# Optimization experiments

Measured on AMD Instinct MI355X. Metric: run time of the kernel, lower is better.

## Reference

```python
import jax, jax.numpy as jnp
import numpy as np

N = 50000   # total nodes in batched graph
E = 400000  # directed edges
G = 512     # number of graphs in batch
F = 128     # input node feature dim
K = 4       # attention heads
H = 64      # hidden feats per head (flatten width = K*H = 256)
EPS = 1e-5  # BatchNorm eps


def _edge_softmax(e, dst, n):
    # softmax of per-edge scores over incoming edges of each dst node; e: [E, K]
    m = jax.ops.segment_max(e, dst, num_segments=n)
    ee = jnp.exp(e - m[dst])
    s = jax.ops.segment_sum(ee, dst, num_segments=n)
    return ee / s[dst]


def _gat_layer(x, W, al, ar, b, resW, src, dst, agg):
    # dgl GATConv with residual=True, LeakyReLU(0.2), bias, ReLU activation
    n = x.shape[0]
    z = (x @ W).reshape(n, K, H)                      # [N, K, H]
    el = jnp.einsum('nkh,kh->nk', z, al)              # [N, K]
    er = jnp.einsum('nkh,kh->nk', z, ar)
    e = jax.nn.leaky_relu(el[src] + er[dst], negative_slope=0.2)  # [E, K]
    a = _edge_softmax(e, dst, n)                      # [E, K]
    rst = jax.ops.segment_sum(a[:, :, None] * z[src], dst, num_segments=n)  # [N, K, H]
    res = (x @ resW).reshape(n, K, H) if resW is not None else x.reshape(n, K, H)
    rst = jax.nn.relu(rst + res + b.reshape(1, K, H))
    return rst.reshape(n, K * H) if agg == 'flatten' else rst.mean(axis=1)


def setup_inputs() -> dict:
    key = jax.random.key(0)
    ks = jax.random.split(key, 16)
    f32 = jnp.float32

    def p(k, shape):
        return jax.random.normal(k, shape, f32) * 0.1

    h = jax.random.normal(ks[0], (N, F), f32)
    src = jax.random.randint(ks[1], (E,), 0, N)
    dst = jax.random.randint(ks[2], (E,), 0, N)
    graph_ids = (jnp.arange(N) * G) // N  # sorted node->graph assignment, all segments nonempty

    return dict(
        h=h, src=src, dst=dst, graph_ids=graph_ids,
        W0=p(ks[3], (F, K * H)), al0=p(ks[4], (K, H)), ar0=p(ks[5], (K, H)),
        b0=jnp.zeros((K * H,), f32), resW0=p(ks[6], (F, K * H)),
        W1=p(ks[7], (K * H, K * H)), al1=p(ks[8], (K, H)), ar1=p(ks[9], (K, H)),
        b1=jnp.zeros((K * H,), f32),
        W2=p(ks[10], (K * H, K * H)), al2=p(ks[11], (K, H)), ar2=p(ks[12], (K, H)),
        b2=jnp.zeros((K * H,), f32),
        Wg=p(ks[13], (H, 1)), bg=jnp.zeros((1,), f32),
        Wm1=p(ks[14], (2 * H, H)), bm1=jnp.zeros((H,), f32),
        bn_g=jnp.ones((H,), f32), bn_b=jnp.zeros((H,), f32),
        bn_m=jnp.zeros((H,), f32), bn_v=jnp.ones((H,), f32),
        Wm2=p(ks[15], (H, 1)), bm2=jnp.zeros((1,), f32),
    )


def reference(h, src, dst, graph_ids, W0, al0, ar0, b0, resW0, W1, al1, ar1, b1,
              W2, al2, ar2, b2, Wg, bg, Wm1, bm1, bn_g, bn_b, bn_m, bn_v, Wm2, bm2):
    # 3 GAT layers: flatten, flatten, mean (dgllife GATPredictor default agg modes)
    x = _gat_layer(h, W0, al0, ar0, b0, resW0, src, dst, 'flatten')   # [N, 256]
    x = _gat_layer(x, W1, al1, ar1, b1, None, src, dst, 'flatten')    # [N, 256] (identity residual)
    x = _gat_layer(x, W2, al2, ar2, b2, None, src, dst, 'mean')       # [N, 64]
    # WeightedSumAndMax readout
    w = jax.nn.sigmoid(x @ Wg + bg)                                   # [N, 1]
    gs = jax.ops.segment_sum(w * x, graph_ids, num_segments=G)        # [G, 64]
    gm = jax.ops.segment_max(x, graph_ids, num_segments=G)            # [G, 64]
    gf = jnp.concatenate([gs, gm], axis=1)                            # [G, 128]
    # MLPPredictor (eval mode: dropout off, BatchNorm uses running stats)
    y = jax.nn.relu(gf @ Wm1 + bm1)
    y = (y - bn_m) / jnp.sqrt(bn_v + EPS) * bn_g + bn_b
    out = jax.nn.sigmoid(y @ Wm2 + bm2)                               # [G, 1]
    return out
```

## Files before the change

kernel.cpp:

```cpp
#include <hip/hip_runtime.h>
#include <math.h>


typedef _Float16 f16;
typedef _Float16 f16x4 __attribute__((ext_vector_type(4)));
typedef _Float16 f16x8 __attribute__((ext_vector_type(8)));
typedef float f32x16 __attribute__((ext_vector_type(16)));

__device__ __forceinline__ double wred_sumd(double v) {
#pragma unroll
  for (int m = 32; m > 0; m >>= 1) v += __shfl_xor(v, m, 64);
  return v;
}
__device__ __forceinline__ float wred_sum(float v) {
#pragma unroll
  for (int m = 32; m > 0; m >>= 1) v += __shfl_xor(v, m, 64);
  return v;
}

__global__ void k_hist(const int* __restrict__ dst, int* __restrict__ deg, int e) {
  int i = blockIdx.x * 256 + threadIdx.x;
  if (i < e) atomicAdd(&deg[dst[i]], 1);
}

__global__ void k_scan1(const int* __restrict__ deg, int* __restrict__ rowptr,
                        int* __restrict__ bsum, int n) {
  __shared__ int sh[256];
  int t = threadIdx.x;
  int base = blockIdx.x * 1024 + t * 4;
  int v0 = 0, v1 = 0, v2 = 0, v3 = 0;
  if (base + 0 < n) v0 = deg[base + 0];
  if (base + 1 < n) v1 = deg[base + 1];
  if (base + 2 < n) v2 = deg[base + 2];
  if (base + 3 < n) v3 = deg[base + 3];
  sh[t] = v0 + v1 + v2 + v3;
  __syncthreads();
  for (int off = 1; off < 256; off <<= 1) {
    int x = (t >= off) ? sh[t - off] : 0;
    __syncthreads();
    sh[t] += x;
    __syncthreads();
  }
  int excl = (t > 0) ? sh[t - 1] : 0;
  if (base + 0 < n) rowptr[base + 0] = excl;
  if (base + 1 < n) rowptr[base + 1] = excl + v0;
  if (base + 2 < n) rowptr[base + 2] = excl + v0 + v1;
  if (base + 3 < n) rowptr[base + 3] = excl + v0 + v1 + v2;
  if (t == 255) bsum[blockIdx.x] = sh[255];
}

__global__ void k_scan2(int* bsum, int nb) {
  if (threadIdx.x == 0 && blockIdx.x == 0) {
    int run = 0;
    for (int i = 0; i < nb; i++) { int v = bsum[i]; bsum[i] = run; run += v; }
  }
}

__global__ void k_scan3(int* __restrict__ rowptr, const int* __restrict__ bsum,
                        int n, int e) {
  int i = blockIdx.x * 256 + threadIdx.x;
  if (i < n) rowptr[i] += bsum[i >> 10];
  if (i == 0) rowptr[n] = e;
}

__global__ void k_scatter(const int* __restrict__ src, const int* __restrict__ dst,
                          const int* __restrict__ rowptr, int* __restrict__ cursor,
                          int* __restrict__ colsrc, int e) {
  int i = blockIdx.x * 256 + threadIdx.x;
  if (i < e) {
    int d = dst[i];
    int pos = rowptr[d] + atomicAdd(&cursor[d], 1);
    colsrc[pos] = src[i];
  }
}

__global__ __launch_bounds__(256) void k_split(const float* __restrict__ X,
                                               f16* __restrict__ X0,
                                               f16* __restrict__ X1, int n4) {
  int i = blockIdx.x * 256 + threadIdx.x;
  if (i >= n4) return;
  float4 v = *(const float4*)(X + (size_t)i * 4);
  f16x4 hi, lo;
  hi.x = (f16)v.x; lo.x = (f16)(v.x - (float)hi.x);
  hi.y = (f16)v.y; lo.y = (f16)(v.y - (float)hi.y);
  hi.z = (f16)v.z; lo.z = (f16)(v.z - (float)hi.z);
  hi.w = (f16)v.w; lo.w = (f16)(v.w - (float)hi.w);
  *(f16x4*)(X0 + (size_t)i * 4) = hi;
  *(f16x4*)(X1 + (size_t)i * 4) = lo;
}

__global__ void k_splitWT(const float* __restrict__ W, f16* __restrict__ P0,
                          f16* __restrict__ P1, int kin) {
  int c = blockIdx.x;
  for (int k = threadIdx.x; k < kin; k += blockDim.x) {
    float v = W[(size_t)k * 256 + c];
    f16 h0 = (f16)v;
    size_t off = ((size_t)(k >> 4) * 256 + c) * 16 + ((k >> 3) & 1) * 8 + (k & 7);
    P0[off] = h0;
    P1[off] = (f16)(v - (float)h0);
  }
}

template <int KIN>
__global__ __launch_bounds__(256) void k_gemm_mfma(
    const f16* __restrict__ X0, const f16* __restrict__ X1,
    const f16* __restrict__ WT0, const f16* __restrict__ WT1,
    float* __restrict__ C, int M) {
  __shared__ f16 aLDS[2][2][64][8];
  const int t = threadIdx.x;
  const int w = t >> 6;
  const int lane = t & 63;
  const int lo = lane & 31, g = lane >> 5;
  const int row0 = blockIdx.x * 32;

  f32x16 acc0, acc1;
#pragma unroll
  for (int i = 0; i < 16; i++) { acc0[i] = 0.f; acc1[i] = 0.f; }

  const size_t fb0 = (size_t)(w * 64 + lo) * 16 + g * 8;
  const size_t fb1 = (size_t)(w * 64 + 32 + lo) * 16 + g * 8;

  for (int k0 = 0; k0 < KIN; k0 += 32) {
    if (k0) __syncthreads();
    {
      int s = t >> 7, r = (t >> 2) & 31, hh = t & 3;
      int kh = hh >> 1, gg = hh & 1;
      int gr = row0 + r;
      if (gr > M - 1) gr = M - 1;
      const f16* Xs = s ? X1 : X0;
      *(float4*)&aLDS[s][kh][(gg << 5) | r][0] =
          *(const float4*)&Xs[(size_t)gr * KIN + k0 + kh * 16 + gg * 8];
    }
    __syncthreads();
#pragma unroll
    for (int kh = 0; kh < 2; kh++) {
      const size_t bbase = (size_t)((k0 >> 4) + kh) * 4096;
      f16x8 a0 = *(const f16x8*)&aLDS[0][kh][lane][0];
      f16x8 a1 = *(const f16x8*)&aLDS[1][kh][lane][0];
      f16x8 b0c0 = *(const f16x8*)&WT0[bbase + fb0];
      f16x8 b0c1 = *(const f16x8*)&WT0[bbase + fb1];
      f16x8 b1c0 = *(const f16x8*)&WT1[bbase + fb0];
      f16x8 b1c1 = *(const f16x8*)&WT1[bbase + fb1];
      acc0 = __builtin_amdgcn_mfma_f32_32x32x16_f16(a0, b0c0, acc0, 0, 0, 0);
      acc1 = __builtin_amdgcn_mfma_f32_32x32x16_f16(a0, b0c1, acc1, 0, 0, 0);
      acc0 = __builtin_amdgcn_mfma_f32_32x32x16_f16(a0, b1c0, acc0, 0, 0, 0);
      acc1 = __builtin_amdgcn_mfma_f32_32x32x16_f16(a0, b1c1, acc1, 0, 0, 0);
      acc0 = __builtin_amdgcn_mfma_f32_32x32x16_f16(a1, b0c0, acc0, 0, 0, 0);
      acc1 = __builtin_amdgcn_mfma_f32_32x32x16_f16(a1, b0c1, acc1, 0, 0, 0);
    }
  }
  const int c0 = w * 64 + lo, c1 = w * 64 + 32 + lo;
#pragma unroll
  for (int reg = 0; reg < 16; reg++) {
    int rr = (reg & 3) + 8 * (reg >> 2) + 4 * g;
    int r0 = row0 + rr;
    if (r0 < M) {
      C[(size_t)r0 * 256 + c0] = acc0[reg];
      C[(size_t)r0 * 256 + c1] = acc1[reg];
    }
  }
}

__global__ __launch_bounds__(256) void k_elr(const float* __restrict__ z,
                                             const float* __restrict__ al,
                                             const float* __restrict__ ar,
                                             float* __restrict__ el,
                                             float* __restrict__ er, int n) {
  int node = blockIdx.x * 4 + (threadIdx.x >> 6);
  int lane = threadIdx.x & 63;
  if (node >= n) return;
  const float* zr = z + (size_t)node * 256;
#pragma unroll
  for (int k = 0; k < 4; k++) {
    float zv = zr[k * 64 + lane];
    float pl = wred_sum(zv * al[k * 64 + lane]);
    float pr = wred_sum(zv * ar[k * 64 + lane]);
    if (lane == 0) {
      el[node * 4 + k] = pl;
      er[node * 4 + k] = pr;
    }
  }
}

template <int MEAN, int RESF16>
__global__ __launch_bounds__(256) void k_gather(
    const float* __restrict__ z, const float* __restrict__ el,
    const float* __restrict__ er, const float* __restrict__ resf,
    const f16* __restrict__ R0, const f16* __restrict__ R1,
    const float* __restrict__ bias, const int* __restrict__ rowptr,
    const int* __restrict__ colsrc, float* __restrict__ out,
    f16* __restrict__ O0, f16* __restrict__ O1, float* __restrict__ wn,
    const float* __restrict__ Wg, const float* __restrict__ bg, int n) {
  const int t = threadIdx.x;
  const int w = t >> 6, lane = t & 63;
  int node = blockIdx.x * 4 + w;
  if (node > n - 1) node = n - 1;
  const int base = rowptr[node];
  const int deg = rowptr[node + 1] - base;
  const int k = lane >> 4, j = lane & 15;
  const float ernk = er[node * 4 + k];

  float m = -INFINITY;
  for (int i0 = 0; i0 < deg; i0 += 16) {
    int i = i0 + j;
    if (i < deg) {
      int s = colsrc[base + i];
      float sc = el[s * 4 + k] + ernk;
      sc = (sc > 0.f) ? sc : 0.2f * sc;
      m = fmaxf(m, sc);
    }
  }
#pragma unroll
  for (int msk = 1; msk < 16; msk <<= 1) m = fmaxf(m, __shfl_xor(m, msk, 64));

  float ssum = 0.f;
  for (int i0 = 0; i0 < deg; i0 += 16) {
    int i = i0 + j;
    if (i < deg) {
      int s = colsrc[base + i];
      float sc = el[s * 4 + k] + ernk;
      sc = (sc > 0.f) ? sc : 0.2f * sc;
      ssum += expf(sc - m);
    }
  }
#pragma unroll
  for (int msk = 1; msk < 16; msk <<= 1) ssum += __shfl_xor(ssum, msk, 64);
  const float inv = 1.f / ssum;

  const char* zb = (const char*)z + lane * 16;
  float4 acc0 = {0, 0, 0, 0}, acc1 = {0, 0, 0, 0};
  float4 acc2 = {0, 0, 0, 0}, acc3 = {0, 0, 0, 0};
  int i = 0;
  for (; i + 4 <= deg; i += 4) {
    int s0 = colsrc[base + i + 0];
    int s1 = colsrc[base + i + 1];
    int s2 = colsrc[base + i + 2];
    int s3 = colsrc[base + i + 3];
    float4 z0 = *(const float4*)(zb + ((size_t)s0 << 10));
    float4 z1 = *(const float4*)(zb + ((size_t)s1 << 10));
    float4 z2 = *(const float4*)(zb + ((size_t)s2 << 10));
    float4 z3 = *(const float4*)(zb + ((size_t)s3 << 10));
    float c0 = el[s0 * 4 + k] + ernk; c0 = (c0 > 0.f) ? c0 : 0.2f * c0;
    float c1 = el[s1 * 4 + k] + ernk; c1 = (c1 > 0.f) ? c1 : 0.2f * c1;
    float c2 = el[s2 * 4 + k] + ernk; c2 = (c2 > 0.f) ? c2 : 0.2f * c2;
    float c3 = el[s3 * 4 + k] + ernk; c3 = (c3 > 0.f) ? c3 : 0.2f * c3;
    float a0 = expf(c0 - m) * inv;
    float a1 = expf(c1 - m) * inv;
    float a2 = expf(c2 - m) * inv;
    float a3 = expf(c3 - m) * inv;
    acc0.x = fmaf(a0, z0.x, acc0.x); acc0.y = fmaf(a0, z0.y, acc0.y);
    acc0.z = fmaf(a0, z0.z, acc0.z); acc0.w = fmaf(a0, z0.w, acc0.w);
    acc1.x = fmaf(a1, z1.x, acc1.x); acc1.y = fmaf(a1, z1.y, acc1.y);
    acc1.z = fmaf(a1, z1.z, acc1.z); acc1.w = fmaf(a1, z1.w, acc1.w);
    acc2.x = fmaf(a2, z2.x, acc2.x); acc2.y = fmaf(a2, z2.y, acc2.y);
    acc2.z = fmaf(a2, z2.z, acc2.z); acc2.w = fmaf(a2, z2.w, acc2.w);
    acc3.x = fmaf(a3, z3.x, acc3.x); acc3.y = fmaf(a3, z3.y, acc3.y);
    acc3.z = fmaf(a3, z3.z, acc3.z); acc3.w = fmaf(a3, z3.w, acc3.w);
  }
  for (; i < deg; i++) {
    int s = colsrc[base + i];
    float4 zv = *(const float4*)(zb + ((size_t)s << 10));
    float c = el[s * 4 + k] + ernk; c = (c > 0.f) ? c : 0.2f * c;
    float av = expf(c - m) * inv;
    acc0.x = fmaf(av, zv.x, acc0.x); acc0.y = fmaf(av, zv.y, acc0.y);
    acc0.z = fmaf(av, zv.z, acc0.z); acc0.w = fmaf(av, zv.w, acc0.w);
  }

  size_t o = (size_t)node * 256 + lane * 4;
  float4 rv;
  if (RESF16) {
    f16x4 rh = *(const f16x4*)(R0 + o);
    f16x4 rl = *(const f16x4*)(R1 + o);
    rv.x = (float)rh.x + (float)rl.x;
    rv.y = (float)rh.y + (float)rl.y;
    rv.z = (float)rh.z + (float)rl.z;
    rv.w = (float)rh.w + (float)rl.w;
  } else {
    rv = *(const float4*)(resf + o);
  }
  float4 bv = *(const float4*)(bias + lane * 4);
  float4 v;
  v.x = fmaxf(((acc0.x + acc1.x) + (acc2.x + acc3.x)) + rv.x + bv.x, 0.f);
  v.y = fmaxf(((acc0.y + acc1.y) + (acc2.y + acc3.y)) + rv.y + bv.y, 0.f);
  v.z = fmaxf(((acc0.z + acc1.z) + (acc2.z + acc3.z)) + rv.z + bv.z, 0.f);
  v.w = fmaxf(((acc0.w + acc1.w) + (acc2.w + acc3.w)) + rv.w + bv.w, 0.f);

  if (!MEAN) {
    f16x4 hi, lo;
    hi.x = (f16)v.x; lo.x = (f16)(v.x - (float)hi.x);
    hi.y = (f16)v.y; lo.y = (f16)(v.y - (float)hi.y);
    hi.z = (f16)v.z; lo.z = (f16)(v.z - (float)hi.z);
    hi.w = (f16)v.w; lo.w = (f16)(v.w - (float)hi.w);
    *(f16x4*)(O0 + o) = hi;
    *(f16x4*)(O1 + o) = lo;
  } else {
    __shared__ float tmp[4][256];
    *(float4*)&tmp[w][lane * 4] = v;
    __syncthreads();
    float xv = 0.25f * (tmp[w][lane] + tmp[w][lane + 64] + tmp[w][lane + 128] +
                        tmp[w][lane + 192]);
    out[(size_t)node * 64 + lane] = xv;
    double s = wred_sumd((double)xv * (double)Wg[lane]);
    if (lane == 0)
      wn[node] = (float)(1.0 / (1.0 + exp(-(s + (double)bg[0]))));
  }
}

__global__ __launch_bounds__(64) void k_readout(const float* __restrict__ x2,
                                                const float* __restrict__ wn,
                                                float* __restrict__ gf, int n,
                                                int g) {
  int gi = blockIdx.x;
  int lane = threadIdx.x;
  long long start = ((long long)gi * n + g - 1) / g;
  long long end = ((long long)(gi + 1) * n + g - 1) / g;
  double s = 0.0;
  float mx = -INFINITY;
  for (long long nd = start; nd < end; nd++) {
    float xv = x2[nd * 64 + lane];
    s += (double)wn[nd] * (double)xv;
    mx = fmaxf(mx, xv);
  }
  gf[gi * 128 + lane] = (float)s;
  gf[gi * 128 + 64 + lane] = mx;
}

__global__ __launch_bounds__(64) void k_mlp(const float* __restrict__ gf,
                                            const float* __restrict__ Wm1,
                                            const float* __restrict__ bm1,
                                            const float* __restrict__ bng,
                                            const float* __restrict__ bnb,
                                            const float* __restrict__ bnm,
                                            const float* __restrict__ bnv,
                                            const float* __restrict__ Wm2,
                                            const float* __restrict__ bm2,
                                            float* __restrict__ out) {
  int gi = blockIdx.x;
  int h = threadIdx.x;
  double y = (double)bm1[h];
  for (int i = 0; i < 128; i++)
    y += (double)gf[gi * 128 + i] * (double)Wm1[i * 64 + h];
  y = (y > 0.0) ? y : 0.0;
  y = (y - (double)bnm[h]) / sqrt((double)bnv[h] + 1e-5) * (double)bng[h] +
      (double)bnb[h];
  double v = wred_sumd(y * (double)Wm2[h]);
  if (h == 0) {
    double s = v + (double)bm2[0];
    out[gi] = (float)(1.0 / (1.0 + exp(-s)));
  }
}

extern "C" void kernel_launch(void* const* d_in, const int* in_sizes, int n_in,
                              void* d_out, int out_size, void* d_ws,
                              size_t ws_size, hipStream_t stream) {
  const float* h    = (const float*)d_in[0];
  const int*   src  = (const int*)d_in[1];
  const int*   dst  = (const int*)d_in[2];
  const float* W0    = (const float*)d_in[4];
  const float* al0   = (const float*)d_in[5];
  const float* ar0   = (const float*)d_in[6];
  const float* b0    = (const float*)d_in[7];
  const float* resW0 = (const float*)d_in[8];
  const float* W1    = (const float*)d_in[9];
  const float* al1   = (const float*)d_in[10];
  const float* ar1   = (const float*)d_in[11];
  const float* b1    = (const float*)d_in[12];
  const float* W2    = (const float*)d_in[13];
  const float* al2   = (const float*)d_in[14];
  const float* ar2   = (const float*)d_in[15];
  const float* b2    = (const float*)d_in[16];
  const float* Wg    = (const float*)d_in[17];
  const float* bg    = (const float*)d_in[18];
  const float* Wm1   = (const float*)d_in[19];
  const float* bm1   = (const float*)d_in[20];
  const float* bng   = (const float*)d_in[21];
  const float* bnb   = (const float*)d_in[22];
  const float* bnm   = (const float*)d_in[23];
  const float* bnv   = (const float*)d_in[24];
  const float* Wm2   = (const float*)d_in[25];
  const float* bm2   = (const float*)d_in[26];

  const int n = in_sizes[0] / 128;
  const int e = in_sizes[1];
  const int g = out_size;

  char* ws = (char*)d_ws;
  size_t off = 0;
  auto alloc = [&](size_t bytes) {
    void* p = ws + off;
    off += (bytes + 255) & ~(size_t)255;
    return p;
  };
  int*   deg    = (int*)alloc((size_t)n * 4);
  int*   cursor = (int*)alloc((size_t)n * 4);
  int*   rowptr = (int*)alloc((size_t)(n + 1) * 4);
  int*   bsum   = (int*)alloc(256 * 4);
  int*   colsrc = (int*)alloc((size_t)e * 4);
  float* el     = (float*)alloc((size_t)n * 4 * 4);
  float* er     = (float*)alloc((size_t)n * 4 * 4);
  float* bufA   = (float*)alloc((size_t)n * 256 * 4);
  float* bufB   = (float*)alloc((size_t)n * 256 * 4);
  float* x2     = (float*)alloc((size_t)n * 64 * 4);
  float* wn     = (float*)alloc((size_t)n * 4);
  float* gf     = (float*)alloc((size_t)g * 128 * 4);
  f16*   sA0    = (f16*)alloc((size_t)n * 256 * 2);
  f16*   sA1    = (f16*)alloc((size_t)n * 256 * 2);
  f16*   sB0    = (f16*)alloc((size_t)n * 256 * 2);
  f16*   sB1    = (f16*)alloc((size_t)n * 256 * 2);
  f16*   wtA0   = (f16*)alloc(65536 * 2);
  f16*   wtA1   = (f16*)alloc(65536 * 2);
  f16*   wtR0   = (f16*)alloc(65536 * 2);
  f16*   wtR1   = (f16*)alloc(65536 * 2);
  f16*   wtB0   = (f16*)alloc(65536 * 2);
  f16*   wtB1   = (f16*)alloc(65536 * 2);
  f16*   wtC0   = (f16*)alloc(65536 * 2);
  f16*   wtC1   = (f16*)alloc(65536 * 2);
  (void)ws_size;
  (void)n_in;

  hipMemsetAsync(deg, 0, (size_t)n * 4, stream);
  hipMemsetAsync(cursor, 0, (size_t)n * 4, stream);

  const int eb = (e + 255) / 256;
  const int nb = (n + 1023) / 1024;
  k_hist<<<eb, 256, 0, stream>>>(dst, deg, e);
  k_scan1<<<nb, 256, 0, stream>>>(deg, rowptr, bsum, n);
  k_scan2<<<1, 64, 0, stream>>>(bsum, nb);
  k_scan3<<<(n + 255) / 256, 256, 0, stream>>>(rowptr, bsum, n, e);
  k_scatter<<<eb, 256, 0, stream>>>(src, dst, rowptr, cursor, colsrc, e);

  k_splitWT<<<256, 256, 0, stream>>>(W0, wtA0, wtA1, 128);
  k_splitWT<<<256, 256, 0, stream>>>(resW0, wtR0, wtR1, 128);
  k_splitWT<<<256, 256, 0, stream>>>(W1, wtB0, wtB1, 256);
  k_splitWT<<<256, 256, 0, stream>>>(W2, wtC0, wtC1, 256);

  const int mb32 = (n + 31) / 32;
  const int n4 = (n + 3) / 4;
  const int sp128 = (n * 128 / 4 + 255) / 256;

  k_split<<<sp128, 256, 0, stream>>>(h, sA0, sA1, n * 128 / 4);
  k_gemm_mfma<128><<<mb32, 256, 0, stream>>>(sA0, sA1, wtA0, wtA1, bufA, n);
  k_gemm_mfma<128><<<mb32, 256, 0, stream>>>(sA0, sA1, wtR0, wtR1, bufB, n);
  k_elr<<<n4, 256, 0, stream>>>(bufA, al0, ar0, el, er, n);
  k_gather<0, 0><<<n4, 256, 0, stream>>>(bufA, el, er, bufB, nullptr, nullptr,
                                         b0, rowptr, colsrc, nullptr, sB0, sB1,
                                         nullptr, nullptr, nullptr, n);

  k_gemm_mfma<256><<<mb32, 256, 0, stream>>>(sB0, sB1, wtB0, wtB1, bufA, n);
  k_elr<<<n4, 256, 0, stream>>>(bufA, al1, ar1, el, er, n);
  k_gather<0, 1><<<n4, 256, 0, stream>>>(bufA, el, er, nullptr, sB0, sB1, b1,
                                         rowptr, colsrc, nullptr, sA0, sA1,
                                         nullptr, nullptr, nullptr, n);

  k_gemm_mfma<256><<<mb32, 256, 0, stream>>>(sA0, sA1, wtC0, wtC1, bufA, n);
  k_elr<<<n4, 256, 0, stream>>>(bufA, al2, ar2, el, er, n);
  k_gather<1, 1><<<n4, 256, 0, stream>>>(bufA, el, er, nullptr, sA0, sA1, b2,
                                         rowptr, colsrc, x2, nullptr, nullptr,
                                         wn, Wg, bg, n);

  k_readout<<<g, 64, 0, stream>>>(x2, wn, gf, n, g);
  k_mlp<<<g, 64, 0, stream>>>(gf, Wm1, bm1, bng, bnb, bnm, bnv, Wm2, bm2,
                              (float*)d_out);
}
```

Before: 515.0 us.

## Fuse attention-logit computation into GEMM epilogue and cache softmax exponentials in LDS

Removes the separate k_elr kernel by computing el/er inside the GEMM after a block barrier, reading the just-written C tile back from memory. In the gather kernel, each edge's exp value from the sum pass is stored in shared memory when degree is at most 128, so the aggregation pass skips re-reading el and recomputing exp. The aggregation loop is also unrolled to 8 independent accumulators for more memory-level parallelism. The costs are extra LDS use per block and a global read-back of C inside the GEMM, which relies on the block's own writes being visible after __syncthreads.

Result: no change. 508.5 us (-1.3%).

```diff
diff --git a/kernel.cpp b/kernel.cpp
--- a/kernel.cpp
+++ b/kernel.cpp
@@ -8,11 +8,6 @@
 typedef float f32x16 __attribute__((ext_vector_type(16)));
 
 __device__ __forceinline__ double wred_sumd(double v) {
-#pragma unroll
-  for (int m = 32; m > 0; m >>= 1) v += __shfl_xor(v, m, 64);
-  return v;
-}
-__device__ __forceinline__ float wred_sum(float v) {
 #pragma unroll
   for (int m = 32; m > 0; m >>= 1) v += __shfl_xor(v, m, 64);
   return v;
@@ -101,11 +96,13 @@
   }
 }
 
-template <int KIN>
+template <int KIN, bool ELR>
 __global__ __launch_bounds__(256) void k_gemm_mfma(
     const f16* __restrict__ X0, const f16* __restrict__ X1,
     const f16* __restrict__ WT0, const f16* __restrict__ WT1,
-    float* __restrict__ C, int M) {
+    float* __restrict__ C, const float* __restrict__ al,
+    const float* __restrict__ ar, float* __restrict__ el,
+    float* __restrict__ er, int M) {
   __shared__ f16 aLDS[2][2][64][8];
   const int t = threadIdx.x;
   const int w = t >> 6;
@@ -159,29 +156,26 @@
       C[(size_t)r0 * 256 + c1] = acc1[reg];
     }
   }
-}
-
-__global__ __launch_bounds__(256) void k_elr(const float* __restrict__ z,
-                                             const float* __restrict__ al,
-                                             const float* __restrict__ ar,
-                                             float* __restrict__ el,
-                                             float* __restrict__ er, int n) {
-  int node = blockIdx.x * 4 + (threadIdx.x >> 6);
-  int lane = threadIdx.x & 63;
-  if (node >= n) return;
-  const float* zr = z + (size_t)node * 256;
-#pragma unroll
-  for (int k = 0; k < 4; k++) {
-    float zv = zr[k * 64 + lane];
-    float pl = wred_sum(zv * al[k * 64 + lane]);
-    float pr = wred_sum(zv * ar[k * 64 + lane]);
-    if (lane == 0) {
-      el[node * 4 + k] = pl;
-      er[node * 4 + k] = pr;
-    }
-  }
-}
-
+  if (ELR) {
+    __syncthreads();
+    int r = t & 31, kk = (t >> 5) & 3, sel = t >> 7;
+    int gr = row0 + r;
+    if (gr < M) {
+      const float* zr = C + (size_t)gr * 256 + kk * 64;
+      const float* av = (sel ? ar : al) + kk * 64;
+      float s = 0.f;
+#pragma unroll
+      for (int q = 0; q < 16; q++) {
+        float4 zv = *(const float4*)(zr + q * 4);
+        float4 a4 = *(const float4*)(av + q * 4);
+        s += zv.x * a4.x + zv.y * a4.y + zv.z * a4.z + zv.w * a4.w;
+      }
+      (sel ? er : el)[gr * 4 + kk] = s;
+    }
+  }
+}
+
+#define SCAP 128
 template <int MEAN, int RESF16>
 __global__ __launch_bounds__(256) void k_gather(
     const float* __restrict__ z, const float* __restrict__ el,
@@ -191,6 +185,7 @@
     const int* __restrict__ colsrc, float* __restrict__ out,
     f16* __restrict__ O0, f16* __restrict__ O1, float* __restrict__ wn,
     const float* __restrict__ Wg, const float* __restrict__ bg, int n) {
+  __shared__ float sExp[4][4][SCAP];
   const int t = threadIdx.x;
   const int w = t >> 6, lane = t & 63;
   int node = blockIdx.x * 4 + w;
@@ -199,6 +194,7 @@
   const int deg = rowptr[node + 1] - base;
   const int k = lane >> 4, j = lane & 15;
   const float ernk = er[node * 4 + k];
+  const bool cached = (deg <= SCAP);
 
   float m = -INFINITY;
   for (int i0 = 0; i0 < deg; i0 += 16) {
@@ -220,7 +216,9 @@
       int s = colsrc[base + i];
       float sc = el[s * 4 + k] + ernk;
       sc = (sc > 0.f) ? sc : 0.2f * sc;
-      ssum += expf(sc - m);
+      float e_ = expf(sc - m);
+      ssum += e_;
+      if (cached) sExp[w][k][i] = e_;
     }
   }
 #pragma unroll
@@ -230,40 +228,46 @@
   const char* zb = (const char*)z + lane * 16;
   float4 acc0 = {0, 0, 0, 0}, acc1 = {0, 0, 0, 0};
   float4 acc2 = {0, 0, 0, 0}, acc3 = {0, 0, 0, 0};
-  int i = 0;
-  for (; i + 4 <= deg; i += 4) {
-    int s0 = colsrc[base + i + 0];
-    int s1 = colsrc[base + i + 1];
-    int s2 = colsrc[base + i + 2];
-    int s3 = colsrc[base + i + 3];
-    float4 z0 = *(const float4*)(zb + ((size_t)s0 << 10));
-    float4 z1 = *(const float4*)(zb + ((size_t)s1 << 10));
-    float4 z2 = *(const float4*)(zb + ((size_t)s2 << 10));
-    float4 z3 = *(const float4*)(zb + ((size_t)s3 << 10));
-    float c0 = el[s0 * 4 + k] + ernk; c0 = (c0 > 0.f) ? c0 : 0.2f * c0;
-    float c1 = el[s1 * 4 + k] + ernk; c1 = (c1 > 0.f) ? c1 : 0.2f * c1;
-    float c2 = el[s2 * 4 + k] + ernk; c2 = (c2 > 0.f) ? c2 : 0.2f * c2;
-    float c3 = el[s3 * 4 + k] + ernk; c3 = (c3 > 0.f) ? c3 : 0.2f * c3;
-    float a0 = expf(c0 - m) * inv;
-    float a1 = expf(c1 - m) * inv;
-    float a2 = expf(c2 - m) * inv;
-    float a3 = expf(c3 - m) * inv;
-    acc0.x = fmaf(a0, z0.x, acc0.x); acc0.y = fmaf(a0, z0.y, acc0.y);
-    acc0.z = fmaf(a0, z0.z, acc0.z); acc0.w = fmaf(a0, z0.w, acc0.w);
-    acc1.x = fmaf(a1, z1.x, acc1.x); acc1.y = fmaf(a1, z1.y, acc1.y);
-    acc1.z = fmaf(a1, z1.z, acc1.z); acc1.w = fmaf(a1, z1.w, acc1.w);
-    acc2.x = fmaf(a2, z2.x, acc2.x); acc2.y = fmaf(a2, z2.y, acc2.y);
-    acc2.z = fmaf(a2, z2.z, acc2.z); acc2.w = fmaf(a2, z2.w, acc2.w);
-    acc3.x = fmaf(a3, z3.x, acc3.x); acc3.y = fmaf(a3, z3.y, acc3.y);
-    acc3.z = fmaf(a3, z3.z, acc3.z); acc3.w = fmaf(a3, z3.w, acc3.w);
-  }
-  for (; i < deg; i++) {
-    int s = colsrc[base + i];
-    float4 zv = *(const float4*)(zb + ((size_t)s << 10));
-    float c = el[s * 4 + k] + ernk; c = (c > 0.f) ? c : 0.2f * c;
-    float av = expf(c - m) * inv;
-    acc0.x = fmaf(av, zv.x, acc0.x); acc0.y = fmaf(av, zv.y, acc0.y);
-    acc0.z = fmaf(av, zv.z, acc0.z); acc0.w = fmaf(av, zv.w, acc0.w);
+  float4 acc4 = {0, 0, 0, 0}, acc5 = {0, 0, 0, 0};
+  float4 acc6 = {0, 0, 0, 0}, acc7 = {0, 0, 0, 0};
+  if (cached) {
+    int i = 0;
+    for (; i + 8 <= deg; i += 8) {
+#pragma unroll
+      for (int q = 0; q < 8; q++) {
+        int s = colsrc[base + i + q];
+        float av = sExp[w][k][i + q] * inv;
+        float4 zv = *(const float4*)(zb + ((size_t)s << 10));
+        float4* ac = (q == 0)   ? &acc0
+                     : (q == 1) ? &acc1
+                     : (q == 2) ? &acc2
+                     : (q == 3) ? &acc3
+                     : (q == 4) ? &acc4
+                     : (q == 5) ? &acc5
+                     : (q == 6) ? &acc6
+                                : &acc7;
+        ac->x = fmaf(av, zv.x, ac->x);
+        ac->y = fmaf(av, zv.y, ac->y);
+        ac->z = fmaf(av, zv.z, ac->z);
+        ac->w = fmaf(av, zv.w, ac->w);
+      }
+    }
+    for (; i < deg; i++) {
+      int s = colsrc[base + i];
+      float av = sExp[w][k][i] * inv;
+      float4 zv = *(const float4*)(zb + ((size_t)s << 10));
+      acc0.x = fmaf(av, zv.x, acc0.x); acc0.y = fmaf(av, zv.y, acc0.y);
+      acc0.z = fmaf(av, zv.z, acc0.z); acc0.w = fmaf(av, zv.w, acc0.w);
+    }
+  } else {
+    for (int i = 0; i < deg; i++) {
+      int s = colsrc[base + i];
+      float4 zv = *(const float4*)(zb + ((size_t)s << 10));
+      float c = el[s * 4 + k] + ernk; c = (c > 0.f) ? c : 0.2f * c;
+      float av = expf(c - m) * inv;
+      acc0.x = fmaf(av, zv.x, acc0.x); acc0.y = fmaf(av, zv.y, acc0.y);
+      acc0.z = fmaf(av, zv.z, acc0.z); acc0.w = fmaf(av, zv.w, acc0.w);
+    }
   }
 
   size_t o = (size_t)node * 256 + lane * 4;
@@ -280,10 +284,14 @@
   }
   float4 bv = *(const float4*)(bias + lane * 4);
   float4 v;
-  v.x = fmaxf(((acc0.x + acc1.x) + (acc2.x + acc3.x)) + rv.x + bv.x, 0.f);
-  v.y = fmaxf(((acc0.y + acc1.y) + (acc2.y + acc3.y)) + rv.y + bv.y, 0.f);
-  v.z = fmaxf(((acc0.z + acc1.z) + (acc2.z + acc3.z)) + rv.z + bv.z, 0.f);
-  v.w = fmaxf(((acc0.w + acc1.w) + (acc2.w + acc3.w)) + rv.w + bv.w, 0.f);
+  v.x = fmaxf((((acc0.x + acc1.x) + (acc2.x + acc3.x)) +
+               ((acc4.x + acc5.x) + (acc6.x + acc7.x))) + rv.x + bv.x, 0.f);
+  v.y = fmaxf((((acc0.y + acc1.y) + (acc2.y + acc3.y)) +
+               ((acc4.y + acc5.y) + (acc6.y + acc7.y))) + rv.y + bv.y, 0.f);
+  v.z = fmaxf((((acc0.z + acc1.z) + (acc2.z + acc3.z)) +
+               ((acc4.z + acc5.z) + (acc6.z + acc7.z))) + rv.z + bv.z, 0.f);
+  v.w = fmaxf((((acc0.w + acc1.w) + (acc2.w + acc3.w)) +
+               ((acc4.w + acc5.w) + (acc6.w + acc7.w))) + rv.w + bv.w, 0.f);
 
   if (!MEAN) {
     f16x4 hi, lo;
@@ -439,21 +447,22 @@
   const int sp128 = (n * 128 / 4 + 255) / 256;
 
   k_split<<<sp128, 256, 0, stream>>>(h, sA0, sA1, n * 128 / 4);
-  k_gemm_mfma<128><<<mb32, 256, 0, stream>>>(sA0, sA1, wtA0, wtA1, bufA, n);
-  k_gemm_mfma<128><<<mb32, 256, 0, stream>>>(sA0, sA1, wtR0, wtR1, bufB, n);
-  k_elr<<<n4, 256, 0, stream>>>(bufA, al0, ar0, el, er, n);
+  k_gemm_mfma<128, true><<<mb32, 256, 0, stream>>>(sA0, sA1, wtA0, wtA1, bufA,
+                                                   al0, ar0, el, er, n);
+  k_gemm_mfma<128, false><<<mb32, 256, 0, stream>>>(
+      sA0, sA1, wtR0, wtR1, bufB, nullptr, nullptr, nullptr, nullptr, n);
   k_gather<0, 0><<<n4, 256, 0, stream>>>(bufA, el, er, bufB, nullptr, nullptr,
                                          b0, rowptr, colsrc, nullptr, sB0, sB1,
                                          nullptr, nullptr, nullptr, n);
 
-  k_gemm_mfma<256><<<mb32, 256, 0, stream>>>(sB0, sB1, wtB0, wtB1, bufA, n);
-  k_elr<<<n4, 256, 0, stream>>>(bufA, al1, ar1, el, er, n);
+  k_gemm_mfma<256, true><<<mb32, 256, 0, stream>>>(sB0, sB1, wtB0, wtB1, bufA,
+                                                   al1, ar1, el, er, n);
   k_gather<0, 1><<<n4, 256, 0, stream>>>(bufA, el, er, nullptr, sB0, sB1, b1,
                                          rowptr, colsrc, nullptr, sA0, sA1,
                                          nullptr, nullptr, nullptr, n);
 
-  k_gemm_mfma<256><<<mb32, 256, 0, stream>>>(sA0, sA1, wtC0, wtC1, bufA, n);
-  k_elr<<<n4, 256, 0, stream>>>(bufA, al2, ar2, el, er, n);
+  k_gemm_mfma<256, true><<<mb32, 256, 0, stream>>>(sA0, sA1, wtC0, wtC1, bufA,
+                                                   al2, ar2, el, er, n);
   k_gather<1, 1><<<n4, 256, 0, stream>>>(bufA, el, er, nullptr, sA0, sA1, b2,
                                          rowptr, colsrc, x2, nullptr, nullptr,
                                          wn, Wg, bg, n);
```
